# Kernel optimization log

Hardware: AMD Instinct MI355X
Metric: run time of the kernel (lower is better)

Reference implementation:

```python
import jax, jax.numpy as jnp
import numpy as np

TAU = 0.1
LAM = 1.0
LOG_NOISE = 1e-12
COS_EPS = 1e-8      # torch CosineSimilarity eps
NORM_EPS = 1e-12    # torch F.normalize eps


def setup_inputs() -> dict:
    key = jax.random.key(0)
    k1, k2, k3, k4 = jax.random.split(key, 4)
    B, D, S = 8192, 128, 64
    z1s = jax.random.normal(k1, (B, D), dtype=jnp.float32)
    z2s = jax.random.normal(k2, (B, D), dtype=jnp.float32)
    z1_c_outs = jax.random.uniform(k3, (B, S), dtype=jnp.float32)
    z1_subject_labels = jax.random.normal(k4, (B, S), dtype=jnp.float32)
    return {"z1s": z1s, "z2s": z2s, "z1_c_outs": z1_c_outs,
            "z1_subject_labels": z1_subject_labels}


def _l2_normalize(x, eps):
    # normalize rows; clamp norm from below like torch
    n = jnp.linalg.norm(x, axis=1, keepdims=True)
    return x / jnp.maximum(n, eps)


def reference(z1s, z2s, z1_c_outs, z1_subject_labels):
    B = z1s.shape[0]
    z1 = z1s.reshape(B, -1)
    z2 = z2s.reshape(B, -1)
    n1 = _l2_normalize(z1, COS_EPS)
    n2 = _l2_normalize(z2, COS_EPS)

    # all-pairs cosine similarities, scaled by temperature
    S12 = jnp.matmul(n1, n2.T) / TAU   # [B, B] sim(z1_i, z2_k)/tau
    S11 = jnp.matmul(n1, n1.T) / TAU   # [B, B] sim(z1_i, z1_k)/tau

    e12 = jnp.exp(S12)
    e11 = jnp.exp(S11)
    numerator = jnp.diagonal(e12)                       # exp(sim(z1_i, z2_i)/tau)
    # denom_i = sum_k e12[i,k] + sum_{k != i} e11[i,k]
    denom = e12.sum(axis=1) + e11.sum(axis=1) - jnp.diagonal(e11)
    contrastive = -jnp.log(LOG_NOISE + numerator / denom)
    loss = contrastive.sum() / (B * (2.0 * B - 1.0))

    # adversarial term: -lam * log(1 - normalized_pred[i, argmax(label_i)])
    c = _l2_normalize(z1_c_outs, NORM_EPS)
    j = jnp.argmax(z1_subject_labels, axis=1)           # [B] int
    picked = c[jnp.arange(B), j]
    loss = loss + LAM * (-jnp.log(LOG_NOISE + 1.0 - picked)).sum()
    return loss
```

## Files before the change

kernel.cpp:

```cpp
#include <hip/hip_runtime.h>
#include <hip/hip_bf16.h>
#include <math.h>


#define NROWS 8192
#define DFEAT 128

typedef __bf16 bf16_t;
typedef __bf16 bf16x8 __attribute__((ext_vector_type(8)));
typedef __bf16 bf16x2 __attribute__((ext_vector_type(2)));
typedef float  f32x4  __attribute__((ext_vector_type(4)));

__device__ __forceinline__ float fexp2(float x) {
#if __has_builtin(__builtin_amdgcn_exp2f)
  return __builtin_amdgcn_exp2f(x);
#else
  return exp2f(x);
#endif
}

__device__ __forceinline__ void stage16(const void* gsrc, void* ldst) {
  __builtin_amdgcn_global_load_lds(
      (const __attribute__((address_space(1))) unsigned int*)gsrc,
      (__attribute__((address_space(3))) unsigned int*)ldst, 16, 0, 0);
}

__global__ __launch_bounds__(1024)
void sa_prep_kernel(const float* __restrict__ z1,
                    const float* __restrict__ z2,
                    bf16_t* __restrict__ Abuf,
                    bf16_t* __restrict__ Kc,
                    float* __restrict__ numv,
                    float* __restrict__ d11v) {
  __shared__ __align__(16) bf16_t LA[16][136];
  __shared__ __align__(16) bf16_t LK2[16][136];
  __shared__ __align__(16) bf16_t LK1[16][136];

  int wave = threadIdx.x >> 6;
  int lane = threadIdx.x & 63;
  int tile = blockIdx.x;
  int row  = tile * 16 + wave;

  float2 a = ((const float2*)(z1 + (size_t)row * DFEAT))[lane];
  float2 b = ((const float2*)(z2 + (size_t)row * DFEAT))[lane];

  float s1  = a.x * a.x + a.y * a.y;
  float s2  = b.x * b.x + b.y * b.y;
  float s12 = a.x * b.x + a.y * b.y;
#pragma unroll
  for (int m = 32; m; m >>= 1) {
    s1  += __shfl_xor(s1, m, 64);
    s2  += __shfl_xor(s2, m, 64);
    s12 += __shfl_xor(s12, m, 64);
  }
  float r1 = 1.0f / fmaxf(sqrtf(s1), 1e-8f);
  float r2 = 1.0f / fmaxf(sqrtf(s2), 1e-8f);

  const float SCL = 14.426950408889634f;

  bf16x2 av;  av[0] = (bf16_t)(a.x * r1 * SCL); av[1] = (bf16_t)(a.y * r1 * SCL);
  bf16x2 k2v; k2v[0] = (bf16_t)(b.x * r2);      k2v[1] = (bf16_t)(b.y * r2);
  bf16x2 k1v; k1v[0] = (bf16_t)(a.x * r1);      k1v[1] = (bf16_t)(a.y * r1);

  *(bf16x2*)&LA[wave][2 * lane]  = av;
  *(bf16x2*)&LK2[wave][2 * lane] = k2v;
  *(bf16x2*)&LK1[wave][2 * lane] = k1v;

  if (lane == 0) {
    numv[row] = expf(10.0f * s12 * r1 * r2);
    d11v[row] = expf(10.0f * s1 * r1 * r1);
  }
  __syncthreads();

  int t = threadIdx.x;
  if (t < 768) {
    int sel = t >> 8;
    int u   = t & 255;
    int kf  = u >> 6;
    int qk  = (u >> 4) & 3;
    int r16 = u & 15;
    const bf16_t* Ls = (sel == 0) ? &LA[0][0]
                     : (sel == 1) ? &LK2[0][0] : &LK1[0][0];
    bf16x8 v = *(const bf16x8*)(Ls + r16 * 136 + kf * 32 + qk * 8);
    bf16_t* dst = (sel == 0) ? (Abuf + (size_t)tile * 2048)
                : (sel == 1) ? (Kc + (size_t)tile * 2048)
                             : (Kc + (size_t)(512 + tile) * 2048);
    *(bf16x8*)(dst + u * 8) = v;
  }
}

__global__ __launch_bounds__(512, 4)
void sa_main_kernel(const bf16_t* __restrict__ Abuf,
                    const bf16_t* __restrict__ Kc,
                    float* __restrict__ T2t) {
  __shared__ __align__(16) bf16_t bsm[32768];

  int wave = threadIdx.x >> 6;
  int lane = threadIdx.x & 63;
  int quad = lane >> 4;

  int id     = blockIdx.x;
  int xcd    = id & 7;
  int within = id >> 3;
  int by     = xcd * 8 + (within >> 4);
  int bx     = within & 15;
  int rowBase = bx * 512 + wave * 64;

  const bf16x8* ap = (const bf16x8*)Abuf + (size_t)(rowBase >> 4) * 256 + lane;
  bf16x8 afrag[4][4];
#pragma unroll
  for (int s = 0; s < 4; ++s)
#pragma unroll
    for (int kfi = 0; kfi < 4; ++kfi)
      afrag[s][kfi] = ap[(s * 4 + kfi) * 64];

  const char* src = (const char*)Kc + (size_t)by * 65536 +
                    (size_t)wave * 8192 + (size_t)lane * 16;
  char* dst = (char*)&bsm[0] + wave * 8192;
#pragma unroll
  for (int i = 0; i < 8; ++i) stage16(src + i * 1024, dst + i * 1024);

  __syncthreads();

  f32x4 sums[4];
#pragma unroll
  for (int s = 0; s < 4; ++s) sums[s] = (f32x4){0.f, 0.f, 0.f, 0.f};

#pragma unroll 1
  for (int i = 0; i < 8; ++i) {
    int p = (wave + i) & 7;
    const bf16_t* base = &bsm[0] + p * 4096;
#pragma unroll
    for (int tt = 0; tt < 2; ++tt) {
      const bf16x8* bs = (const bf16x8*)(base + tt * 2048);
      bf16x8 bfr[4];
#pragma unroll
      for (int kfi = 0; kfi < 4; ++kfi) bfr[kfi] = bs[kfi * 64 + lane];
#pragma unroll
      for (int s = 0; s < 4; ++s) {
        f32x4 c = {0.f, 0.f, 0.f, 0.f};
        __builtin_amdgcn_s_setprio(1);
#pragma unroll
        for (int kfi = 0; kfi < 4; ++kfi)
          c = __builtin_amdgcn_mfma_f32_16x16x32_bf16(afrag[s][kfi], bfr[kfi],
                                                      c, 0, 0, 0);
        __builtin_amdgcn_s_setprio(0);
#pragma unroll
        for (int r = 0; r < 4; ++r) sums[s][r] += fexp2(c[r]);
      }
    }
  }

  int l15 = lane & 15;
#pragma unroll
  for (int s = 0; s < 4; ++s) {
    f32x4 st;
#pragma unroll
    for (int r = 0; r < 4; ++r) {
      float v = sums[s][r];
      v += __shfl_xor(v, 1, 64);
      v += __shfl_xor(v, 2, 64);
      v += __shfl_xor(v, 4, 64);
      v += __shfl_xor(v, 8, 64);
      st[r] = v;
    }
    if (l15 == 0)
      *(f32x4*)(T2t + (size_t)by * 8192 + rowBase + s * 16 + quad * 4) = st;
  }
}

__global__ __launch_bounds__(256)
void sa_final_adv_kernel(const float* __restrict__ T2t,
                         const float* __restrict__ numv,
                         const float* __restrict__ d11v,
                         const float* __restrict__ c,
                         const float* __restrict__ lab,
                         float* __restrict__ partial) {
  int wave = threadIdx.x >> 6;
  int lane = threadIdx.x & 63;
  int row  = blockIdx.x * 4 + wave;

  float cv = c[row * 64 + lane];
  float lv = lab[row * 64 + lane];
  float tv = T2t[(size_t)lane * 8192 + row];

  float ss = cv * cv;
  float bestv = lv;
  int   besti = lane;
#pragma unroll
  for (int m = 32; m; m >>= 1) {
    ss += __shfl_xor(ss, m, 64);
    tv += __shfl_xor(tv, m, 64);
    float ov = __shfl_xor(bestv, m, 64);
    int   oi = __shfl_xor(besti, m, 64);
    if (ov > bestv || (ov == bestv && oi < besti)) { bestv = ov; besti = oi; }
  }
  float picked = __shfl(cv, besti, 64) / fmaxf(sqrtf(ss), 1e-12f);

  float term = 0.0f;
  if (lane == 0) {
    float denom = tv - d11v[row];
    term = -logf(1e-12f + numv[row] / denom) * (1.0f / 134209536.0f)
           - logf(1e-12f + 1.0f - picked);
  }

  __shared__ float wacc[4];
  if (lane == 0) wacc[wave] = term;
  __syncthreads();
  if (threadIdx.x == 0)
    partial[blockIdx.x] = wacc[0] + wacc[1] + wacc[2] + wacc[3];
}

__global__ __launch_bounds__(256)
void sa_reduce_kernel(const float* __restrict__ partial,
                      float* __restrict__ out) {
  float v = 0.0f;
#pragma unroll
  for (int i = 0; i < 8; ++i) v += partial[threadIdx.x + 256 * i];
#pragma unroll
  for (int m = 32; m; m >>= 1) v += __shfl_xor(v, m, 64);
  __shared__ float wacc[4];
  if ((threadIdx.x & 63) == 0) wacc[threadIdx.x >> 6] = v;
  __syncthreads();
  if (threadIdx.x == 0) out[0] = wacc[0] + wacc[1] + wacc[2] + wacc[3];
}

extern "C" void kernel_launch(void* const* d_in, const int* in_sizes, int n_in,
                              void* d_out, int out_size, void* d_ws,
                              size_t ws_size, hipStream_t stream) {
  const float* z1  = (const float*)d_in[0];
  const float* z2  = (const float*)d_in[1];
  const float* co  = (const float*)d_in[2];
  const float* lab = (const float*)d_in[3];
  float* out = (float*)d_out;

  char* ws = (char*)d_ws;
  bf16_t* Abuf  = (bf16_t*)ws;
  bf16_t* Kc    = (bf16_t*)(ws + 2u * 1024 * 1024);
  float*  T2t   = (float*)(ws + 6u * 1024 * 1024);
  float*  numv  = (float*)(ws + 8u * 1024 * 1024);
  float*  d11v  = numv + NROWS;
  float*  part  = d11v + NROWS;

  sa_prep_kernel<<<NROWS / 16, 1024, 0, stream>>>(z1, z2, Abuf, Kc, numv,
                                                  d11v);
  sa_main_kernel<<<1024, 512, 0, stream>>>(Abuf, Kc, T2t);
  sa_final_adv_kernel<<<NROWS / 4, 256, 0, stream>>>(T2t, numv, d11v, co, lab,
                                                     part);
  sa_reduce_kernel<<<1, 256, 0, stream>>>(part, out);
}
```

Baseline: 106.0 us.

## Switch main similarity GEMM to 32x32x16 MFMA with 32-row tiles

Replaces the 16x16x32 bf16 MFMA tiling with the 32x32x16 instruction. Each wave now owns 32 query rows instead of 64, and the grid doubles to 2048 blocks. The prep kernel is reworked to emit 32-row fragment layouts matching the new operand format. The larger MFMA shape is meant to cut LDS B-fragment reads per FLOP and improve matrix-core throughput, but it halves the per-wave A reuse and doubles the block count and K-tile staging traffic.

```diff
diff --git a/kernel.cpp b/kernel.cpp
--- a/kernel.cpp
+++ b/kernel.cpp
@@ -10,6 +10,7 @@
 typedef __bf16 bf16x8 __attribute__((ext_vector_type(8)));
 typedef __bf16 bf16x2 __attribute__((ext_vector_type(2)));
 typedef float  f32x4  __attribute__((ext_vector_type(4)));
+typedef float  f32x16 __attribute__((ext_vector_type(16)));
 
 __device__ __forceinline__ float fexp2(float x) {
 #if __has_builtin(__builtin_amdgcn_exp2f)
@@ -32,60 +33,63 @@
                     bf16_t* __restrict__ Kc,
                     float* __restrict__ numv,
                     float* __restrict__ d11v) {
-  __shared__ __align__(16) bf16_t LA[16][136];
-  __shared__ __align__(16) bf16_t LK2[16][136];
-  __shared__ __align__(16) bf16_t LK1[16][136];
+  __shared__ __align__(16) bf16_t L[3][32][136];
 
   int wave = threadIdx.x >> 6;
   int lane = threadIdx.x & 63;
-  int tile = blockIdx.x;
-  int row  = tile * 16 + wave;
-
-  float2 a = ((const float2*)(z1 + (size_t)row * DFEAT))[lane];
-  float2 b = ((const float2*)(z2 + (size_t)row * DFEAT))[lane];
-
-  float s1  = a.x * a.x + a.y * a.y;
-  float s2  = b.x * b.x + b.y * b.y;
-  float s12 = a.x * b.x + a.y * b.y;
-#pragma unroll
-  for (int m = 32; m; m >>= 1) {
-    s1  += __shfl_xor(s1, m, 64);
-    s2  += __shfl_xor(s2, m, 64);
-    s12 += __shfl_xor(s12, m, 64);
-  }
-  float r1 = 1.0f / fmaxf(sqrtf(s1), 1e-8f);
-  float r2 = 1.0f / fmaxf(sqrtf(s2), 1e-8f);
+  int blk  = blockIdx.x;
 
   const float SCL = 14.426950408889634f;
 
-  bf16x2 av;  av[0] = (bf16_t)(a.x * r1 * SCL); av[1] = (bf16_t)(a.y * r1 * SCL);
-  bf16x2 k2v; k2v[0] = (bf16_t)(b.x * r2);      k2v[1] = (bf16_t)(b.y * r2);
-  bf16x2 k1v; k1v[0] = (bf16_t)(a.x * r1);      k1v[1] = (bf16_t)(a.y * r1);
-
-  *(bf16x2*)&LA[wave][2 * lane]  = av;
-  *(bf16x2*)&LK2[wave][2 * lane] = k2v;
-  *(bf16x2*)&LK1[wave][2 * lane] = k1v;
-
-  if (lane == 0) {
-    numv[row] = expf(10.0f * s12 * r1 * r2);
-    d11v[row] = expf(10.0f * s1 * r1 * r1);
-  }
-  __syncthreads();
-
-  int t = threadIdx.x;
-  if (t < 768) {
-    int sel = t >> 8;
-    int u   = t & 255;
-    int kf  = u >> 6;
-    int qk  = (u >> 4) & 3;
-    int r16 = u & 15;
-    const bf16_t* Ls = (sel == 0) ? &LA[0][0]
-                     : (sel == 1) ? &LK2[0][0] : &LK1[0][0];
-    bf16x8 v = *(const bf16x8*)(Ls + r16 * 136 + kf * 32 + qk * 8);
-    bf16_t* dst = (sel == 0) ? (Abuf + (size_t)tile * 2048)
-                : (sel == 1) ? (Kc + (size_t)tile * 2048)
-                             : (Kc + (size_t)(512 + tile) * 2048);
-    *(bf16x8*)(dst + u * 8) = v;
+#pragma unroll
+  for (int r = 0; r < 2; ++r) {
+    int rl  = wave * 2 + r;
+    int row = blk * 32 + rl;
+
+    float2 a = ((const float2*)(z1 + (size_t)row * DFEAT))[lane];
+    float2 b = ((const float2*)(z2 + (size_t)row * DFEAT))[lane];
+
+    float s1  = a.x * a.x + a.y * a.y;
+    float s2  = b.x * b.x + b.y * b.y;
+    float s12 = a.x * b.x + a.y * b.y;
+#pragma unroll
+    for (int m = 32; m; m >>= 1) {
+      s1  += __shfl_xor(s1, m, 64);
+      s2  += __shfl_xor(s2, m, 64);
+      s12 += __shfl_xor(s12, m, 64);
+    }
+    float r1 = 1.0f / fmaxf(sqrtf(s1), 1e-8f);
+    float r2 = 1.0f / fmaxf(sqrtf(s2), 1e-8f);
+
+    bf16x2 av;  av[0] = (bf16_t)(a.x * r1 * SCL); av[1] = (bf16_t)(a.y * r1 * SCL);
+    bf16x2 k2v; k2v[0] = (bf16_t)(b.x * r2);      k2v[1] = (bf16_t)(b.y * r2);
+    bf16x2 k1v; k1v[0] = (bf16_t)(a.x * r1);      k1v[1] = (bf16_t)(a.y * r1);
+
+    *(bf16x2*)&L[0][rl][2 * lane] = av;
+    *(bf16x2*)&L[1][rl][2 * lane] = k2v;
+    *(bf16x2*)&L[2][rl][2 * lane] = k1v;
+
+    if (lane == 0) {
+      numv[row] = expf(10.0f * s12 * r1 * r2);
+      d11v[row] = expf(10.0f * s1 * r1 * r1);
+    }
+  }
+  __syncthreads();
+
+#pragma unroll
+  for (int st = 0; st < 2; ++st) {
+    int t = threadIdx.x + st * 1024;
+    if (t < 1536) {
+      int sel = t >> 9;
+      int u   = t & 511;
+      int lu  = u & 63;
+      int kf  = u >> 6;
+      bf16x8 v = *(const bf16x8*)&L[sel][lu & 31][kf * 16 + (lu >> 5) * 8];
+      bf16_t* dst = (sel == 0) ? (Abuf + (size_t)blk * 4096)
+                  : (sel == 1) ? (Kc + (size_t)blk * 4096)
+                               : (Kc + (size_t)(256 + blk) * 4096);
+      *(bf16x8*)(dst + u * 8) = v;
+    }
   }
 }
 
@@ -97,22 +101,18 @@
 
   int wave = threadIdx.x >> 6;
   int lane = threadIdx.x & 63;
-  int quad = lane >> 4;
 
   int id     = blockIdx.x;
   int xcd    = id & 7;
   int within = id >> 3;
-  int by     = xcd * 8 + (within >> 4);
-  int bx     = within & 15;
-  int rowBase = bx * 512 + wave * 64;
-
-  const bf16x8* ap = (const bf16x8*)Abuf + (size_t)(rowBase >> 4) * 256 + lane;
-  bf16x8 afrag[4][4];
-#pragma unroll
-  for (int s = 0; s < 4; ++s)
-#pragma unroll
-    for (int kfi = 0; kfi < 4; ++kfi)
-      afrag[s][kfi] = ap[(s * 4 + kfi) * 64];
+  int by     = xcd * 8 + (within >> 5);
+  int bx     = within & 31;
+  int rowBase = bx * 256 + wave * 32;
+
+  const bf16x8* ap = (const bf16x8*)Abuf + (size_t)(bx * 8 + wave) * 512 + lane;
+  bf16x8 afrag[8];
+#pragma unroll
+  for (int kf = 0; kf < 8; ++kf) afrag[kf] = ap[kf * 64];
 
   const char* src = (const char*)Kc + (size_t)by * 65536 +
                     (size_t)wave * 8192 + (size_t)lane * 16;
@@ -122,50 +122,48 @@
 
   __syncthreads();
 
-  f32x4 sums[4];
-#pragma unroll
-  for (int s = 0; s < 4; ++s) sums[s] = (f32x4){0.f, 0.f, 0.f, 0.f};
+  float sums[16];
+#pragma unroll
+  for (int r = 0; r < 16; ++r) sums[r] = 0.0f;
 
 #pragma unroll 1
   for (int i = 0; i < 8; ++i) {
     int p = (wave + i) & 7;
-    const bf16_t* base = &bsm[0] + p * 4096;
-#pragma unroll
-    for (int tt = 0; tt < 2; ++tt) {
-      const bf16x8* bs = (const bf16x8*)(base + tt * 2048);
-      bf16x8 bfr[4];
-#pragma unroll
-      for (int kfi = 0; kfi < 4; ++kfi) bfr[kfi] = bs[kfi * 64 + lane];
-#pragma unroll
-      for (int s = 0; s < 4; ++s) {
-        f32x4 c = {0.f, 0.f, 0.f, 0.f};
-        __builtin_amdgcn_s_setprio(1);
-#pragma unroll
-        for (int kfi = 0; kfi < 4; ++kfi)
-          c = __builtin_amdgcn_mfma_f32_16x16x32_bf16(afrag[s][kfi], bfr[kfi],
-                                                      c, 0, 0, 0);
-        __builtin_amdgcn_s_setprio(0);
-#pragma unroll
-        for (int r = 0; r < 4; ++r) sums[s][r] += fexp2(c[r]);
-      }
-    }
-  }
-
-  int l15 = lane & 15;
-#pragma unroll
-  for (int s = 0; s < 4; ++s) {
-    f32x4 st;
-#pragma unroll
-    for (int r = 0; r < 4; ++r) {
-      float v = sums[s][r];
-      v += __shfl_xor(v, 1, 64);
-      v += __shfl_xor(v, 2, 64);
-      v += __shfl_xor(v, 4, 64);
-      v += __shfl_xor(v, 8, 64);
-      st[r] = v;
-    }
-    if (l15 == 0)
-      *(f32x4*)(T2t + (size_t)by * 8192 + rowBase + s * 16 + quad * 4) = st;
+    const bf16x8* bs = (const bf16x8*)&bsm[0] + p * 512 + lane;
+    bf16x8 bfr[8];
+#pragma unroll
+    for (int kf = 0; kf < 8; ++kf) bfr[kf] = bs[kf * 64];
+
+    f32x16 c = (f32x16)(0.0f);
+    __builtin_amdgcn_s_setprio(1);
+#pragma unroll
+    for (int kf = 0; kf < 8; ++kf)
+      c = __builtin_amdgcn_mfma_f32_32x32x16_bf16(afrag[kf], bfr[kf], c,
+                                                  0, 0, 0);
+    __builtin_amdgcn_s_setprio(0);
+#pragma unroll
+    for (int r = 0; r < 16; ++r) sums[r] += fexp2(c[r]);
+  }
+
+#pragma unroll
+  for (int r = 0; r < 16; ++r) {
+    float v = sums[r];
+    v += __shfl_xor(v, 1, 64);
+    v += __shfl_xor(v, 2, 64);
+    v += __shfl_xor(v, 4, 64);
+    v += __shfl_xor(v, 8, 64);
+    v += __shfl_xor(v, 16, 64);
+    sums[r] = v;
+  }
+  if ((lane & 31) == 0) {
+    int h = lane >> 5;
+    float* base = T2t + (size_t)by * 8192 + rowBase;
+#pragma unroll
+    for (int g = 0; g < 4; ++g) {
+      f32x4 st = {sums[4 * g], sums[4 * g + 1], sums[4 * g + 2],
+                  sums[4 * g + 3]};
+      *(f32x4*)(base + 8 * g + 4 * h) = st;
+    }
   }
 }
 
@@ -242,9 +240,9 @@
   float*  d11v  = numv + NROWS;
   float*  part  = d11v + NROWS;
 
-  sa_prep_kernel<<<NROWS / 16, 1024, 0, stream>>>(z1, z2, Abuf, Kc, numv,
+  sa_prep_kernel<<<NROWS / 32, 1024, 0, stream>>>(z1, z2, Abuf, Kc, numv,
                                                   d11v);
-  sa_main_kernel<<<1024, 512, 0, stream>>>(Abuf, Kc, T2t);
+  sa_main_kernel<<<2048, 512, 0, stream>>>(Abuf, Kc, T2t);
   sa_final_adv_kernel<<<NROWS / 4, 256, 0, stream>>>(T2t, numv, d11v, co, lab,
                                                      part);
   sa_reduce_kernel<<<1, 256, 0, stream>>>(part, out);
```

Result: slower. 119.6 us (+12.9%).

## Halve rows per wave and software-pipeline MFMA with exp accumulation

Applied to the files above, without the earlier changes.

Each block now covers 256 rows instead of 512, with 32 rows per wave, and the grid doubles to 2048 blocks. The inner loop is restructured into a double-buffered pipeline: the LDS load and MFMA for the next B tile are issued before the exp2 accumulation of the previous tile, so exp work on the VALU can overlap matrix-core work. The setprio hints are dropped. The cost is that each block reuses the staged K tile across fewer rows, so total LDS staging traffic doubles. It also adds register pressure from the two buffers.

```diff
diff --git a/kernel.cpp b/kernel.cpp
--- a/kernel.cpp
+++ b/kernel.cpp
@@ -102,14 +102,14 @@
   int id     = blockIdx.x;
   int xcd    = id & 7;
   int within = id >> 3;
-  int by     = xcd * 8 + (within >> 4);
-  int bx     = within & 15;
-  int rowBase = bx * 512 + wave * 64;
+  int by     = xcd * 8 + (within >> 5);
+  int bx     = within & 31;
+  int rowBase = bx * 256 + wave * 32;
 
   const bf16x8* ap = (const bf16x8*)Abuf + (size_t)(rowBase >> 4) * 256 + lane;
-  bf16x8 afrag[4][4];
-#pragma unroll
-  for (int s = 0; s < 4; ++s)
+  bf16x8 afrag[2][4];
+#pragma unroll
+  for (int s = 0; s < 2; ++s)
 #pragma unroll
     for (int kfi = 0; kfi < 4; ++kfi)
       afrag[s][kfi] = ap[(s * 4 + kfi) * 64];
@@ -122,38 +122,57 @@
 
   __syncthreads();
 
-  f32x4 sums[4];
-#pragma unroll
-  for (int s = 0; s < 4; ++s) sums[s] = (f32x4){0.f, 0.f, 0.f, 0.f};
-
+  f32x4 sums[2];
+#pragma unroll
+  for (int s = 0; s < 2; ++s) sums[s] = (f32x4){0.f, 0.f, 0.f, 0.f};
+
+  auto ldb = [&](int g, bf16x8 (&bfr)[4]) {
+    int p = (wave + (g >> 1)) & 7;
+    const bf16x8* bs =
+        (const bf16x8*)(&bsm[0] + p * 4096 + (g & 1) * 2048);
+#pragma unroll
+    for (int kfi = 0; kfi < 4; ++kfi) bfr[kfi] = bs[kfi * 64 + lane];
+  };
+  auto mm = [&](const bf16x8 (&bfr)[4], f32x4 (&c)[2]) {
+#pragma unroll
+    for (int s = 0; s < 2; ++s) {
+      f32x4 acc = {0.f, 0.f, 0.f, 0.f};
+#pragma unroll
+      for (int kfi = 0; kfi < 4; ++kfi)
+        acc = __builtin_amdgcn_mfma_f32_16x16x32_bf16(afrag[s][kfi], bfr[kfi],
+                                                      acc, 0, 0, 0);
+      c[s] = acc;
+    }
+  };
+  auto ex = [&](const f32x4 (&c)[2]) {
+#pragma unroll
+    for (int s = 0; s < 2; ++s)
+#pragma unroll
+      for (int r = 0; r < 4; ++r) sums[s][r] += fexp2(c[s][r]);
+  };
+
+  bf16x8 bA[4], bB[4];
+  f32x4 cA[2], cB[2];
+
+  ldb(0, bA);
+  mm(bA, cA);
 #pragma unroll 1
-  for (int i = 0; i < 8; ++i) {
-    int p = (wave + i) & 7;
-    const bf16_t* base = &bsm[0] + p * 4096;
-#pragma unroll
-    for (int tt = 0; tt < 2; ++tt) {
-      const bf16x8* bs = (const bf16x8*)(base + tt * 2048);
-      bf16x8 bfr[4];
-#pragma unroll
-      for (int kfi = 0; kfi < 4; ++kfi) bfr[kfi] = bs[kfi * 64 + lane];
-#pragma unroll
-      for (int s = 0; s < 4; ++s) {
-        f32x4 c = {0.f, 0.f, 0.f, 0.f};
-        __builtin_amdgcn_s_setprio(1);
-#pragma unroll
-        for (int kfi = 0; kfi < 4; ++kfi)
-          c = __builtin_amdgcn_mfma_f32_16x16x32_bf16(afrag[s][kfi], bfr[kfi],
-                                                      c, 0, 0, 0);
-        __builtin_amdgcn_s_setprio(0);
-#pragma unroll
-        for (int r = 0; r < 4; ++r) sums[s][r] += fexp2(c[r]);
-      }
-    }
-  }
+  for (int g = 1; g <= 13; g += 2) {
+    ldb(g, bB);
+    mm(bB, cB);
+    ex(cA);
+    ldb(g + 1, bA);
+    mm(bA, cA);
+    ex(cB);
+  }
+  ldb(15, bB);
+  mm(bB, cB);
+  ex(cA);
+  ex(cB);
 
   int l15 = lane & 15;
 #pragma unroll
-  for (int s = 0; s < 4; ++s) {
+  for (int s = 0; s < 2; ++s) {
     f32x4 st;
 #pragma unroll
     for (int r = 0; r < 4; ++r) {
@@ -244,7 +263,7 @@
 
   sa_prep_kernel<<<NROWS / 16, 1024, 0, stream>>>(z1, z2, Abuf, Kc, numv,
                                                   d11v);
-  sa_main_kernel<<<1024, 512, 0, stream>>>(Abuf, Kc, T2t);
+  sa_main_kernel<<<2048, 512, 0, stream>>>(Abuf, Kc, T2t);
   sa_final_adv_kernel<<<NROWS / 4, 256, 0, stream>>>(T2t, numv, d11v, co, lab,
                                                      part);
   sa_reduce_kernel<<<1, 256, 0, stream>>>(part, out);
```

Result: slower. 111.2 us (+4.9%).
